# Performance work log

Measured on AMD Instinct MI355X. Metric: run time of the kernel, lower is better.

The kernel has to match this reference:

```python
import jax, jax.numpy as jnp
import numpy as np

B = 128          # graphs
N = 512          # nodes per graph
NT = B * N       # total nodes = 65536
E = NT * 16      # total edges = 1048576
IN = 64
H = 128
OUT = 2
L = 4            # num_layers
RATIO = 0.8


def setup_inputs() -> dict:
    key = jax.random.key(0)
    ks = jax.random.split(key, 20)

    def w(k, shape, fan_in):
        return jax.random.normal(k, shape, jnp.float32) / np.sqrt(fan_in)

    x = jax.random.normal(ks[0], (NT, IN), jnp.float32)
    edge_index = jax.random.randint(ks[1], (2, E), 0, NT, dtype=jnp.int32)
    batch = (jnp.arange(NT) // N).astype(jnp.int32)  # equal-size graphs

    return {
        "x": x,
        "edge_index": edge_index,
        "batch": batch,
        # conv1: GraphConv(IN, H, aggr='mean') -> lin_rel (w/ bias) + lin_root (no bias)
        "W1_rel": w(ks[2], (IN, H), IN),
        "W1_root": w(ks[3], (IN, H), IN),
        "b1": jnp.zeros((H,), jnp.float32),
        # convs[0..2]: GraphConv(H, H, aggr='mean'), stacked
        "Wc_rel": w(ks[4], (L - 1, H, H), H),
        "Wc_root": w(ks[5], (L - 1, H, H), H),
        "bc": jnp.zeros((L - 1, H), jnp.float32),
        # SAGPooling score GNN: GraphConv(H, 1) with default aggr='add'
        "pw_rel": w(ks[6], (H,), H),
        "pw_root": w(ks[7], (H,), H),
        "pb": jnp.zeros((1,), jnp.float32),
        # MLP head
        "lin1_W": w(ks[8], (L * H, H), L * H),
        "lin1_b": jnp.zeros((H,), jnp.float32),
        "lin2_W": w(ks[9], (H, OUT), H),
        "lin2_b": jnp.zeros((OUT,), jnp.float32),
    }


def _graph_conv_mean(x, src, dst, emask, W_rel, W_root, b, n):
    # PyG GraphConv: lin_rel(mean_{j->i} x_j) + lin_root(x_i); masked edges excluded.
    msg = x[src] * emask[:, None]                                  # [E, D] gather
    s = jax.ops.segment_sum(msg, dst, num_segments=n)              # [n, D] scatter-add
    cnt = jax.ops.segment_sum(emask, dst, num_segments=n)          # [n]
    agg = s / jnp.maximum(cnt, 1.0)[:, None]                       # zero for isolated nodes
    return agg @ W_rel + x @ W_root + b


def reference(x, edge_index, batch, W1_rel, W1_root, b1, Wc_rel, Wc_root, bc,
              pw_rel, pw_root, pb, lin1_W, lin1_b, lin2_W, lin2_b):
    src = edge_index[0]
    dst = edge_index[1]
    emask = jnp.ones((E,), jnp.float32)
    n = NT
    npg = N  # nodes per graph (all graphs equal size)

    h = jax.nn.relu(_graph_conv_mean(x, src, dst, emask, W1_rel, W1_root, b1, n))
    xs = [h.reshape(B, npg, H).mean(axis=1)]  # global_mean_pool

    for i in range(L - 1):
        h = jax.nn.relu(_graph_conv_mean(h, src, dst, emask, Wc_rel[i], Wc_root[i], bc[i], n))
        xs.append(h.reshape(B, npg, H).mean(axis=1))
        if i % 2 == 0 and i < L - 2:
            # ---- SAGPooling: score via GraphConv(H,1) with add aggregation ----
            smsg = jax.ops.segment_sum(h[src] * emask[:, None], dst, num_segments=n)
            score = smsg @ pw_rel + h @ pw_root + pb[0]            # [n]
            k = int(np.ceil(RATIO * npg))
            topv, topi = jax.lax.top_k(score.reshape(B, npg), k)   # per-graph top-k
            perm = (jnp.arange(B)[:, None] * npg + topi).reshape(-1)  # global kept ids
            h = h[perm] * jnp.tanh(topv.reshape(-1))[:, None]
            # remap edges; edges touching dropped nodes get masked out
            node_map = jnp.full((n,), -1, jnp.int32).at[perm].set(
                jnp.arange(B * k, dtype=jnp.int32))
            ns, nd = node_map[src], node_map[dst]
            keep = ((ns >= 0) & (nd >= 0)).astype(jnp.float32)
            emask = emask * keep
            src = jnp.where(ns >= 0, ns, 0)
            dst = jnp.where(nd >= 0, nd, 0)
            n = B * k
            npg = k

    xcat = jnp.concatenate(xs, axis=-1)                            # JumpingKnowledge 'cat'
    out = jax.nn.relu(xcat @ lin1_W + lin1_b)
    # dropout is identity in eval mode
    out = out @ lin2_W + lin2_b
    return jax.nn.log_softmax(out, axis=-1)
```

## Files before the change

kernel.cpp:

```cpp
#include <hip/hip_runtime.h>
#include <math.h>

#define NT 65536
#define EE 1048576
#define NB 128
#define KK 410
#define HH 128

typedef short bf16x8 __attribute__((ext_vector_type(8)));
typedef float f32x4 __attribute__((ext_vector_type(4)));
typedef unsigned int u32x4 __attribute__((ext_vector_type(4)));

__device__ __align__(16) unsigned short g_xbs[(size_t)8 * NT * 8];
__device__ __align__(16) unsigned short g_hs1[(size_t)8 * NT * 16];
__device__ __align__(16) unsigned short g_hgs[(size_t)8 * NT * 16];
__device__ __align__(16) unsigned short g_hb2[(size_t)NT * HH];
__device__ __align__(16) unsigned char  g_h8b[(size_t)8 * NT * 16];
__device__ __align__(16) unsigned short g_agg[(size_t)16 * NT * 8];
__device__ __align__(16) unsigned short g_wt1[128 * 128];
__device__ __align__(16) unsigned short g_wtc[3 * 128 * 256];
__device__ __align__(16) unsigned short g_csr1u[EE];
__device__ unsigned short g_keptu[NT];
__device__ unsigned int g_ebuck[EE];
__device__ int g_bcnt[128];
__device__ int g_bbase[129];
__device__ int g_bcur[128];
__device__ int g_nperm[NT];
__device__ float g_trel[NT];
__device__ float g_troot[NT];
__device__ float g_gatef[NT];
__device__ float g_kinv[NT];
__device__ float g_xc4[4 * NB * 4 * 128];
__device__ int g_rows1[NT + 1];

__device__ __forceinline__ unsigned short* wbuf(int id) { return id ? g_wtc : g_wt1; }

__device__ __forceinline__ float b2f(unsigned short u) {
    union { unsigned int i; float f; } v;
    v.i = ((unsigned int)u) << 16;
    return v.f;
}
__device__ __forceinline__ unsigned short f2b(float f) {
    unsigned int x = __float_as_uint(f);
    unsigned int r = x + 0x7fffu + ((x >> 16) & 1u);
    return (unsigned short)(r >> 16);
}
__device__ __forceinline__ unsigned int pk2(float a, float b) {
    return (unsigned int)f2b(a) | ((unsigned int)f2b(b) << 16);
}
__device__ __forceinline__ unsigned int mul2(unsigned int wd, float g) {
    float lo = b2f((unsigned short)(wd & 0xffffu)) * g;
    float hi = b2f((unsigned short)(wd >> 16)) * g;
    return pk2(lo, hi);
}
__device__ __forceinline__ unsigned char enc8(float v) {
    v = fminf(v, 496.0f);
    unsigned int b = __float_as_uint(v * 0x1p-120f);
    unsigned int r = (b + 0x3ffffu + ((b >> 19) & 1u)) >> 19;
    return (unsigned char)r;
}
#define DEC8(u) ((u) ? __uint_as_float(((unsigned int)(u) << 19) + 0x3C000000u) : 0.0f)

__global__ void k_prep(const float* __restrict__ x,
                       const float* __restrict__ W1r, const float* __restrict__ W1o,
                       const float* __restrict__ Wcr, const float* __restrict__ Wco) {
    int tid = blockIdx.x * 256 + threadIdx.x;
    if (tid < 1048576) {
        float4 v = *(const float4*)&x[(size_t)tid * 4];
        unsigned int lo = pk2(v.x, v.y);
        unsigned int hi = pk2(v.z, v.w);
        int node = tid >> 4;
        int sl = (tid & 15) >> 1;
        int of = (tid & 1) * 4;
        *(uint2*)&g_xbs[(((size_t)sl) * NT + node) * 8 + of] = make_uint2(lo, hi);
    } else if (tid < 1048576 + 16384) {
        int r = tid - 1048576;
        int k = r & 127, n = r >> 7;
        float v = (k < 64) ? W1r[k * 128 + n] : W1o[(k - 64) * 128 + n];
        g_wt1[n * 128 + k] = f2b(v);
    } else if (tid < 1048576 + 16384 + 98304) {
        int r = tid - (1048576 + 16384);
        int l = r >> 15;
        int k = r & 255, n = (r >> 8) & 127;
        float v = (k < 128) ? Wcr[l * 16384 + k * 128 + n]
                            : Wco[l * 16384 + (k - 128) * 128 + n];
        g_wtc[l * 32768 + n * 256 + k] = f2b(v);
    } else if (tid < 1048576 + 16384 + 98304 + 128) {
        g_bcnt[tid - (1048576 + 16384 + 98304)] = 0;
    }
}

__global__ __launch_bounds__(256) void k_bhist(const int* __restrict__ dst) {
    __shared__ int h[128];
    if (threadIdx.x < 128) h[threadIdx.x] = 0;
    __syncthreads();
    int e0 = (blockIdx.x * 256 + threadIdx.x) * 4;
    int4 d = *(const int4*)&dst[e0];
    atomicAdd(&h[d.x >> 9], 1);
    atomicAdd(&h[d.y >> 9], 1);
    atomicAdd(&h[d.z >> 9], 1);
    atomicAdd(&h[d.w >> 9], 1);
    __syncthreads();
    if (threadIdx.x < 128 && h[threadIdx.x]) atomicAdd(&g_bcnt[threadIdx.x], h[threadIdx.x]);
}

__global__ __launch_bounds__(128) void k_bscan() {
    __shared__ int s[128];
    int t = threadIdx.x;
    int v = g_bcnt[t];
    s[t] = v;
    __syncthreads();
    for (int off = 1; off < 128; off <<= 1) {
        int u = (t >= off) ? s[t - off] : 0;
        __syncthreads();
        s[t] += u;
        __syncthreads();
    }
    g_bbase[t] = s[t] - v;
    g_bcur[t] = s[t] - v;
    if (t == 127) g_bbase[128] = s[127];
}

__global__ __launch_bounds__(256) void k_bscatter(const int* __restrict__ src,
                                                  const int* __restrict__ dst) {
    __shared__ int h[128];
    __shared__ int base[128];
    if (threadIdx.x < 128) h[threadIdx.x] = 0;
    __syncthreads();
    int e0 = (blockIdx.x * 256 + threadIdx.x) * 4;
    int4 s = *(const int4*)&src[e0];
    int4 d = *(const int4*)&dst[e0];
    int b0 = d.x >> 9, b1 = d.y >> 9, b2 = d.z >> 9, b3 = d.w >> 9;
    atomicAdd(&h[b0], 1);
    atomicAdd(&h[b1], 1);
    atomicAdd(&h[b2], 1);
    atomicAdd(&h[b3], 1);
    __syncthreads();
    if (threadIdx.x < 128) {
        int c = h[threadIdx.x];
        base[threadIdx.x] = c ? atomicAdd(&g_bcur[threadIdx.x], c) : 0;
        h[threadIdx.x] = 0;
    }
    __syncthreads();
    int r0 = atomicAdd(&h[b0], 1);
    g_ebuck[base[b0] + r0] = ((unsigned int)(d.x & 511) << 16) | (unsigned int)s.x;
    int r1 = atomicAdd(&h[b1], 1);
    g_ebuck[base[b1] + r1] = ((unsigned int)(d.y & 511) << 16) | (unsigned int)s.y;
    int r2 = atomicAdd(&h[b2], 1);
    g_ebuck[base[b2] + r2] = ((unsigned int)(d.z & 511) << 16) | (unsigned int)s.z;
    int r3 = atomicAdd(&h[b3], 1);
    g_ebuck[base[b3] + r3] = ((unsigned int)(d.w & 511) << 16) | (unsigned int)s.w;
}

__global__ __launch_bounds__(512) void k_bcsr() {
    __shared__ int hist[512];
    __shared__ int offs[512];
    __shared__ int cur[512];
    int g = blockIdx.x, t = threadIdx.x;
    hist[t] = 0;
    cur[t] = 0;
    __syncthreads();
    int b0 = g_bbase[g], b1 = g_bbase[g + 1];
    for (int e = b0 + t; e < b1; e += 512) {
        unsigned int p = g_ebuck[e];
        atomicAdd(&hist[p >> 16], 1);
    }
    __syncthreads();
    int v = hist[t];
    offs[t] = v;
    __syncthreads();
    for (int off = 1; off < 512; off <<= 1) {
        int u = (t >= off) ? offs[t - off] : 0;
        __syncthreads();
        offs[t] += u;
        __syncthreads();
    }
    int excl = offs[t] - v;
    g_rows1[g * 512 + t] = b0 + excl;
    if (t == 511) g_rows1[g * 512 + 512] = b0 + excl + v;
    __syncthreads();
    offs[t] = excl;
    __syncthreads();
    for (int e = b0 + t; e < b1; e += 512) {
        unsigned int p = g_ebuck[e];
        int dl = p >> 16;
        int r = atomicAdd(&cur[dl], 1);
        g_csr1u[b0 + offs[dl] + r] = (unsigned short)(p & 0xFFFFu);
    }
}

__global__ __launch_bounds__(512) void k_dperm() {
    __shared__ int h[64];
    __shared__ int base[64];
    int g = blockIdx.x, t = threadIdx.x;
    if (t < 64) h[t] = 0;
    __syncthreads();
    int n = g * 512 + t;
    int d = min(g_rows1[n + 1] - g_rows1[n], 63);
    atomicAdd(&h[d], 1);
    __syncthreads();
    if (t == 0) {
        int ss = 0;
        for (int i = 0; i < 64; i++) { base[i] = ss; ss += h[i]; }
    }
    __syncthreads();
    int pos = atomicAdd(&base[d], 1);
    g_nperm[g * 512 + pos] = n;
}

#define ACCP(wd, J) { acc[J] += b2f((unsigned short)((wd) & 0xffffu)); acc[(J) + 1] += b2f((unsigned short)((wd) >> 16)); }
#define ACCQ(q, B) ACCP(q.x, B) ACCP(q.y, (B) + 2) ACCP(q.z, (B) + 4) ACCP(q.w, (B) + 6)

template <int F, int DEN, int FP8>
__global__ __launch_bounds__(256) void k_agg(int srcId) {
    int s = blockIdx.x & 7;
    int idx = (blockIdx.x >> 3) * 256 + threadIdx.x;
    int node = g_nperm[idx];
    const unsigned short* sp = nullptr;
    const unsigned char* sp8 = nullptr;
    if constexpr (FP8) {
        sp8 = g_h8b + (size_t)s * NT * 16;
    } else if constexpr (F == 8) {
        sp = g_xbs + (size_t)s * NT * 8;
    } else {
        sp = (srcId == 0 ? g_hs1 : g_hgs) + (size_t)s * NT * 16;
    }
    int r0 = g_rows1[node], r1 = g_rows1[node + 1];
    float inv;
    if (DEN) {
        inv = g_kinv[node];
    } else {
        int c = r1 - r0;
        inv = 1.0f / (float)(c > 0 ? c : 1);
    }
    constexpr int NA = FP8 ? 16 : F;
    float acc[NA];
#pragma unroll
    for (int i = 0; i < NA; i++) acc[i] = 0.f;

    auto body = [&](int ii) {
        if constexpr (FP8) {
            uint4 w = *(const uint4*)&sp8[(size_t)ii * 16];
            acc[0] += DEC8(w.x & 0xffu);
            acc[1] += DEC8((w.x >> 8) & 0xffu);
            acc[2] += DEC8((w.x >> 16) & 0xffu);
            acc[3] += DEC8(w.x >> 24);
            acc[4] += DEC8(w.y & 0xffu);
            acc[5] += DEC8((w.y >> 8) & 0xffu);
            acc[6] += DEC8((w.y >> 16) & 0xffu);
            acc[7] += DEC8(w.y >> 24);
            acc[8] += DEC8(w.z & 0xffu);
            acc[9] += DEC8((w.z >> 8) & 0xffu);
            acc[10] += DEC8((w.z >> 16) & 0xffu);
            acc[11] += DEC8(w.z >> 24);
            acc[12] += DEC8(w.w & 0xffu);
            acc[13] += DEC8((w.w >> 8) & 0xffu);
            acc[14] += DEC8((w.w >> 16) & 0xffu);
            acc[15] += DEC8(w.w >> 24);
        } else if constexpr (F == 8) {
            uint4 v = *(const uint4*)&sp[(size_t)ii * 8];
            ACCQ(v, 0)
        } else {
            uint4 v = *(const uint4*)&sp[(size_t)ii * 16];
            uint4 v2 = *(const uint4*)&sp[(size_t)ii * 16 + 8];
            ACCQ(v, 0) ACCQ(v2, 8)
        }
    };

    int e = r0;
    for (; e < r1 && (e & 3); e++) body((int)g_csr1u[e]);
    for (; e + 4 <= r1; e += 4) {
        uint2 iv = *(const uint2*)&g_csr1u[e];
        body((int)(iv.x & 0xffffu));
        body((int)(iv.x >> 16));
        body((int)(iv.y & 0xffffu));
        body((int)(iv.y >> 16));
    }
    for (; e < r1; e++) body((int)g_csr1u[e]);

    int gb0 = (NA == 8) ? s : 2 * s;
    u32x4 o;
    o[0] = pk2(acc[0] * inv, acc[1] * inv);
    o[1] = pk2(acc[2] * inv, acc[3] * inv);
    o[2] = pk2(acc[4] * inv, acc[5] * inv);
    o[3] = pk2(acc[6] * inv, acc[7] * inv);
    __builtin_nontemporal_store(o, (u32x4*)&g_agg[((size_t)gb0 * NT + node) * 8]);
    if constexpr (NA == 16) {
        u32x4 o2;
        o2[0] = pk2(acc[8] * inv, acc[9] * inv);
        o2[1] = pk2(acc[10] * inv, acc[11] * inv);
        o2[2] = pk2(acc[12] * inv, acc[13] * inv);
        o2[3] = pk2(acc[14] * inv, acc[15] * inv);
        __builtin_nontemporal_store(o2, (u32x4*)&g_agg[((size_t)(gb0 + 1) * NT + node) * 8]);
    }
}

__global__ __launch_bounds__(256) void k_kinv() {
    int node = blockIdx.x * 256 + threadIdx.x;
    int r0 = g_rows1[node], r1 = g_rows1[node + 1];
    int kc = 0;
    int e = r0;
    for (; e < r1 && (e & 3); e++) kc += (int)g_keptu[g_csr1u[e]];
    for (; e + 4 <= r1; e += 4) {
        uint2 iv = *(const uint2*)&g_csr1u[e];
        kc += (int)g_keptu[iv.x & 0xffffu] + (int)g_keptu[iv.x >> 16]
            + (int)g_keptu[iv.y & 0xffffu] + (int)g_keptu[iv.y >> 16];
    }
    for (; e < r1; e++) kc += (int)g_keptu[g_csr1u[e]];
    g_kinv[node] = 1.0f / (float)(kc > 0 ? kc : 1);
}

__global__ __launch_bounds__(256) void k_gateS() {
    int tid = blockIdx.x * 256 + threadIdx.x;
    int n = tid >> 3, s = tid & 7;
    float g = g_gatef[n];
    const unsigned short* srcp = &g_hb2[(size_t)n * 128 + s * 16];
    uint4 a = *(const uint4*)srcp;
    uint4 b = *(const uint4*)(srcp + 8);
    uint4 oa, ob;
    oa.x = mul2(a.x, g); oa.y = mul2(a.y, g); oa.z = mul2(a.z, g); oa.w = mul2(a.w, g);
    ob.x = mul2(b.x, g); ob.y = mul2(b.y, g); ob.z = mul2(b.z, g); ob.w = mul2(b.w, g);
    unsigned short* d = &g_hgs[((size_t)s * NT + n) * 16];
    *(uint4*)d = oa;
    *(uint4*)(d + 8) = ob;
}

template <int KA, int KB, int MASKED, int DOTS, int ROOTK, int OUTK>
__global__ __launch_bounds__(256) void k_mm(int wsel, int wOfs,
                                            int rootSel,
                                            const float* __restrict__ bias, int sec,
                                            const float* __restrict__ pwr,
                                            const float* __restrict__ pwt) {
    __shared__ float s[128];
    __shared__ unsigned short t16[(OUTK >= 2) ? 128 * 136 : 2];
    const unsigned short* Wt = wbuf(wsel) + wOfs;
    const unsigned short* sb = (ROOTK == 1) ? (rootSel ? g_hgs : g_hs1) : g_xbs;
    int rowbase = blockIdx.x * 128;
    const int K = KA + KB;
    int lane = threadIdx.x & 63;
    int w = threadIdx.x >> 6;
    int n16 = lane & 15, quad = lane >> 4;
    int rowloc = w * 32;
    int rowg = rowbase + rowloc;
    int g = blockIdx.x >> 2, qb = blockIdx.x & 3;
    f32x4 acc[2][8];
#pragma unroll
    for (int rt = 0; rt < 2; rt++)
#pragma unroll
        for (int ct = 0; ct < 8; ct++)
#pragma unroll
            for (int i = 0; i < 4; i++) acc[rt][ct][i] = 0.f;

#pragma unroll
    for (int ks = 0; ks < K / 32; ks++) {
        int k0 = ks * 32;
        bf16x8 a0, a1;
        if (k0 < KA) {
            int fg = (k0 + quad * 8) >> 3;
            a0 = *(const bf16x8*)&g_agg[((size_t)fg * NT + rowg + n16) * 8];
            a1 = *(const bf16x8*)&g_agg[((size_t)fg * NT + rowg + 16 + n16) * 8];
        } else {
            int col = k0 - KA + quad * 8;
            if constexpr (ROOTK == 0) {
                int fg = col >> 3;
                a0 = *(const bf16x8*)&g_xbs[((size_t)fg * NT + rowg + n16) * 8];
                a1 = *(const bf16x8*)&g_xbs[((size_t)fg * NT + rowg + 16 + n16) * 8];
            } else {
                int fg = col >> 4, off = col & 15;
                a0 = *(const bf16x8*)&sb[((size_t)fg * NT + rowg + n16) * 16 + off];
                a1 = *(const bf16x8*)&sb[((size_t)fg * NT + rowg + 16 + n16) * 16 + off];
            }
        }
#pragma unroll
        for (int ct = 0; ct < 8; ct++) {
            bf16x8 b = *(const bf16x8*)&Wt[(size_t)(ct * 16 + n16) * K + k0 + quad * 8];
            acc[0][ct] = __builtin_amdgcn_mfma_f32_16x16x32_bf16(a0, b, acc[0][ct], 0, 0, 0);
            acc[1][ct] = __builtin_amdgcn_mfma_f32_16x16x32_bf16(a1, b, acc[1][ct], 0, 0, 0);
        }
    }

    if (threadIdx.x < 128) s[threadIdx.x] = 0.f;
#pragma unroll
    for (int rt = 0; rt < 2; rt++) {
        float m[4];
#pragma unroll
        for (int i = 0; i < 4; i++) {
            int r = rowg + rt * 16 + quad * 4 + i;
            m[i] = (!MASKED || g_keptu[r]) ? 1.0f : 0.0f;
        }
#pragma unroll
        for (int ct = 0; ct < 8; ct++) {
            int c = ct * 16 + n16;
            float bv = bias[c];
#pragma unroll
            for (int i = 0; i < 4; i++) {
                int r = rowg + rt * 16 + quad * 4 + i;
                float v = fmaxf(acc[rt][ct][i] + bv, 0.f) * m[i];
                acc[rt][ct][i] = v;
                if constexpr (OUTK == 1) g_hb2[(size_t)r * 128 + c] = f2b(v);
                if constexpr (OUTK >= 2) t16[(rowloc + rt * 16 + quad * 4 + i) * 136 + c] = f2b(v);
            }
        }
    }
    __syncthreads();

#pragma unroll
    for (int ct = 0; ct < 8; ct++) {
        float p = 0.f;
#pragma unroll
        for (int rt = 0; rt < 2; rt++)
#pragma unroll
            for (int i = 0; i < 4; i++) p += acc[rt][ct][i];
        p += __shfl_xor(p, 16);
        p += __shfl_xor(p, 32);
        if (quad == 0) atomicAdd(&s[ct * 16 + n16], p);
    }

    if (DOTS) {
        float pr[8], pt[8];
#pragma unroll
        for (int ct = 0; ct < 8; ct++) {
            pr[ct] = pwr[ct * 16 + n16];
            pt[ct] = pwt[ct * 16 + n16];
        }
#pragma unroll
        for (int rt = 0; rt < 2; rt++)
#pragma unroll
            for (int i = 0; i < 4; i++) {
                float dr = 0.f, dt = 0.f;
#pragma unroll
                for (int ct = 0; ct < 8; ct++) {
                    dr += acc[rt][ct][i] * pr[ct];
                    dt += acc[rt][ct][i] * pt[ct];
                }
                dr += __shfl_xor(dr, 1); dt += __shfl_xor(dt, 1);
                dr += __shfl_xor(dr, 2); dt += __shfl_xor(dt, 2);
                dr += __shfl_xor(dr, 4); dt += __shfl_xor(dt, 4);
                dr += __shfl_xor(dr, 8); dt += __shfl_xor(dt, 8);
                if (n16 == 0) {
                    int r = rowg + rt * 16 + quad * 4 + i;
                    g_trel[r] = dr;
                    g_troot[r] = dt;
                }
            }
    }
    __syncthreads();
    if (threadIdx.x < 128)
        g_xc4[((sec * NB + g) * 4 + qb) * 128 + threadIdx.x] = s[threadIdx.x];

    if constexpr (OUTK >= 2) {
        int tid = threadIdx.x;
#pragma unroll
        for (int rep = 0; rep < 8; rep++) {
            int chunk = rep * 256 + tid;
            int s_ = chunk >> 8, rem = chunk & 255;
            int nl = rem >> 1, hf = rem & 1;
            bf16x8 val = *(const bf16x8*)&t16[nl * 136 + s_ * 16 + hf * 8];
            *(bf16x8*)&g_hs1[((size_t)s_ * NT + rowbase + nl) * 16 + hf * 8] = val;
        }
        if constexpr (OUTK == 3) {
#pragma unroll
            for (int rep = 0; rep < 4; rep++) {
                int chunk = rep * 256 + tid;
                int s_ = chunk >> 7, nl = chunk & 127;
                const unsigned short* p = &t16[nl * 136 + s_ * 16];
                unsigned int wq[4];
#pragma unroll
                for (int q = 0; q < 4; q++) {
                    unsigned int c0 = enc8(b2f(p[q * 4 + 0]));
                    unsigned int c1 = enc8(b2f(p[q * 4 + 1]));
                    unsigned int c2 = enc8(b2f(p[q * 4 + 2]));
                    unsigned int c3 = enc8(b2f(p[q * 4 + 3]));
                    wq[q] = c0 | (c1 << 8) | (c2 << 16) | (c3 << 24);
                }
                *(uint4*)&g_h8b[((size_t)s_ * NT + rowbase + nl) * 16] =
                    make_uint4(wq[0], wq[1], wq[2], wq[3]);
            }
        }
    }
}

__global__ __launch_bounds__(256) void k_topk(const float* __restrict__ pb) {
    __shared__ float sv[512];
    __shared__ int si[512];
    int g = blockIdx.x, t = threadIdx.x;
    float pbv = pb[0];
    for (int l = t; l < 512; l += 256) {
        int node = g * 512 + l;
        int r0 = g_rows1[node], r1 = g_rows1[node + 1];
        float s = 0.f;
        int e = r0;
        for (; e + 4 <= r1; e += 4) {
            float s0 = g_trel[g_csr1u[e]];
            float s1 = g_trel[g_csr1u[e + 1]];
            float s2 = g_trel[g_csr1u[e + 2]];
            float s3 = g_trel[g_csr1u[e + 3]];
            s += (s0 + s1) + (s2 + s3);
        }
        for (; e < r1; e++) s += g_trel[g_csr1u[e]];
        sv[l] = s + g_troot[node] + pbv;
        si[l] = l;
    }
    __syncthreads();
    for (int k = 2; k <= 512; k <<= 1) {
        for (int j = k >> 1; j > 0; j >>= 1) {
            for (int i = t; i < 512; i += 256) {
                int p = i ^ j;
                if (p > i) {
                    float va = sv[i], vb = sv[p];
                    int ia = si[i], ib = si[p];
                    bool aFirst = (va > vb) || (va == vb && ia < ib);
                    bool up = ((i & k) == 0);
                    if (up != aFirst) { sv[i] = vb; sv[p] = va; si[i] = ib; si[p] = ia; }
                }
            }
            __syncthreads();
        }
    }
    for (int r = t; r < 512; r += 256) {
        int old = g * 512 + si[r];
        if (r < KK) {
            g_gatef[old] = tanhf(sv[r]);
            g_keptu[old] = 1;
        } else {
            g_gatef[old] = 0.f;
            g_keptu[old] = 0;
        }
    }
}

__global__ __launch_bounds__(128) void k_head(const float* __restrict__ W1, const float* __restrict__ b1,
                                              const float* __restrict__ W2, const float* __restrict__ b2,
                                              float* __restrict__ out) {
    __shared__ float xr[512];
    __shared__ float r0[128], r1[128];
    int g = blockIdx.x, t = threadIdx.x;
    for (int i = t; i < 512; i += 128) {
        int sec = i >> 7, c = i & 127;
        const float* p = &g_xc4[((sec * NB + g) * 4) * 128 + c];
        float v = p[0] + p[128] + p[256] + p[384];
        float inv = (sec < 2) ? (1.0f / 512.0f) : (1.0f / 410.0f);
        xr[i] = v * inv;
    }
    __syncthreads();
    float acc = b1[t];
    for (int k = 0; k < 512; k++) acc += xr[k] * W1[k * 128 + t];
    acc = fmaxf(acc, 0.f);
    r0[t] = acc * W2[t * 2 + 0];
    r1[t] = acc * W2[t * 2 + 1];
    __syncthreads();
    for (int off = 64; off > 0; off >>= 1) {
        if (t < off) { r0[t] += r0[t + off]; r1[t] += r1[t + off]; }
        __syncthreads();
    }
    if (t == 0) {
        float z0 = r0[0] + b2[0], z1 = r1[0] + b2[1];
        float m = fmaxf(z0, z1);
        float l = m + logf(expf(z0 - m) + expf(z1 - m));
        out[g * 2 + 0] = z0 - l;
        out[g * 2 + 1] = z1 - l;
    }
}

extern "C" void kernel_launch(void* const* d_in, const int* in_sizes, int n_in,
                              void* d_out, int out_size, void* d_ws, size_t ws_size,
                              hipStream_t stream) {
    const float* x = (const float*)d_in[0];
    const int* ei = (const int*)d_in[1];
    const int* src = ei;
    const int* dst = ei + EE;
    const float* W1r = (const float*)d_in[3];
    const float* W1o = (const float*)d_in[4];
    const float* b1 = (const float*)d_in[5];
    const float* Wcr = (const float*)d_in[6];
    const float* Wco = (const float*)d_in[7];
    const float* bc = (const float*)d_in[8];
    const float* pwr = (const float*)d_in[9];
    const float* pwt = (const float*)d_in[10];
    const float* pb = (const float*)d_in[11];
    const float* l1W = (const float*)d_in[12];
    const float* l1b = (const float*)d_in[13];
    const float* l2W = (const float*)d_in[14];
    const float* l2b = (const float*)d_in[15];
    float* out = (float*)d_out;

    k_prep<<<(1048576 + 16384 + 98304 + 128 + 255) / 256, 256, 0, stream>>>(x, W1r, W1o, Wcr, Wco);

    k_bhist<<<1024, 256, 0, stream>>>(dst);
    k_bscan<<<1, 128, 0, stream>>>();
    k_bscatter<<<1024, 256, 0, stream>>>(src, dst);
    k_bcsr<<<128, 512, 0, stream>>>();
    k_dperm<<<NB, 512, 0, stream>>>();

    k_agg<8, 0, 0><<<2048, 256, 0, stream>>>(0);
    k_mm<64, 64, 0, 0, 0, 2><<<512, 256, 0, stream>>>(0, 0, 0, b1, 0, pwr, pwt);

    k_agg<16, 0, 0><<<2048, 256, 0, stream>>>(0);
    k_mm<128, 128, 0, 1, 1, 1><<<512, 256, 0, stream>>>(1, 0, 0, bc, 1, pwr, pwt);

    k_topk<<<NB, 256, 0, stream>>>(pb);
    k_kinv<<<NT / 256, 256, 0, stream>>>();
    k_gateS<<<2048, 256, 0, stream>>>();

    k_agg<16, 1, 0><<<2048, 256, 0, stream>>>(1);
    k_mm<128, 128, 1, 0, 1, 3><<<512, 256, 0, stream>>>(1, 32768, 1, bc + 128, 2, pwr, pwt);

    k_agg<16, 1, 1><<<2048, 256, 0, stream>>>(0);
    k_mm<128, 128, 1, 0, 1, 0><<<512, 256, 0, stream>>>(1, 65536, 0, bc + 256, 3, pwr, pwt);

    k_head<<<NB, 128, 0, stream>>>(l1W, l1b, l2W, l2b, out);
}
```

Measured before the change: 531.1 us.

## Sort nodes by degree inside aggregation blocks and split 16-wide rows across two lanes

The separate k_dperm kernel and its global permutation array are removed. Each aggregation block now builds its own degree-sorted node order in shared memory. For the bf16 16-feature aggregation passes, each node row is split across two threads, each loading 8 features, and the grid is doubled. This cuts per-thread register use and serial latency per edge and adds parallelism, at the cost of duplicate CSR index reads per pair of lanes and the in-block sort overhead.

```diff
diff --git a/kernel.cpp b/kernel.cpp
--- a/kernel.cpp
+++ b/kernel.cpp
@@ -25,15 +25,12 @@
 __device__ int g_bcnt[128];
 __device__ int g_bbase[129];
 __device__ int g_bcur[128];
-__device__ int g_nperm[NT];
 __device__ float g_trel[NT];
 __device__ float g_troot[NT];
 __device__ float g_gatef[NT];
 __device__ float g_kinv[NT];
 __device__ float g_xc4[4 * NB * 4 * 128];
 __device__ int g_rows1[NT + 1];
-
-__device__ __forceinline__ unsigned short* wbuf(int id) { return id ? g_wtc : g_wt1; }
 
 __device__ __forceinline__ float b2f(unsigned short u) {
     union { unsigned int i; float f; } v;
@@ -189,33 +186,41 @@
     }
 }
 
-__global__ __launch_bounds__(512) void k_dperm() {
-    __shared__ int h[64];
-    __shared__ int base[64];
-    int g = blockIdx.x, t = threadIdx.x;
-    if (t < 64) h[t] = 0;
-    __syncthreads();
-    int n = g * 512 + t;
-    int d = min(g_rows1[n + 1] - g_rows1[n], 63);
-    atomicAdd(&h[d], 1);
+template <int F, int DEN, int FP8, int LPR>
+__global__ __launch_bounds__(256) void k_agg(int srcId) {
+    constexpr int NPB = 256 / LPR;
+    __shared__ int dh[64];
+    __shared__ int db[64];
+    __shared__ unsigned short sord[NPB];
+    int s = blockIdx.x & 7;
+    int nodebase = (blockIdx.x >> 3) * NPB;
+    int t = threadIdx.x;
+
+    if (t < 64) dh[t] = 0;
+    __syncthreads();
+    int dcap = 0;
+    if (t < NPB) {
+        int n = nodebase + t;
+        dcap = min(g_rows1[n + 1] - g_rows1[n], 63);
+        atomicAdd(&dh[dcap], 1);
+    }
     __syncthreads();
     if (t == 0) {
         int ss = 0;
-        for (int i = 0; i < 64; i++) { base[i] = ss; ss += h[i]; }
-    }
-    __syncthreads();
-    int pos = atomicAdd(&base[d], 1);
-    g_nperm[g * 512 + pos] = n;
-}
-
-#define ACCP(wd, J) { acc[J] += b2f((unsigned short)((wd) & 0xffffu)); acc[(J) + 1] += b2f((unsigned short)((wd) >> 16)); }
-#define ACCQ(q, B) ACCP(q.x, B) ACCP(q.y, (B) + 2) ACCP(q.z, (B) + 4) ACCP(q.w, (B) + 6)
-
-template <int F, int DEN, int FP8>
-__global__ __launch_bounds__(256) void k_agg(int srcId) {
-    int s = blockIdx.x & 7;
-    int idx = (blockIdx.x >> 3) * 256 + threadIdx.x;
-    int node = g_nperm[idx];
+#pragma unroll
+        for (int i = 0; i < 64; i++) { db[i] = ss; ss += dh[i]; }
+    }
+    __syncthreads();
+    if (t < NPB) {
+        int p = atomicAdd(&db[dcap], 1);
+        sord[p] = (unsigned short)t;
+    }
+    __syncthreads();
+
+    int row = sord[t / LPR];
+    int half = (LPR == 2) ? (t & 1) : 0;
+    int node = nodebase + row;
+
     const unsigned short* sp = nullptr;
     const unsigned char* sp8 = nullptr;
     if constexpr (FP8) {
@@ -223,7 +228,7 @@
     } else if constexpr (F == 8) {
         sp = g_xbs + (size_t)s * NT * 8;
     } else {
-        sp = (srcId == 0 ? g_hs1 : g_hgs) + (size_t)s * NT * 16;
+        sp = (srcId == 0 ? g_hs1 : g_hgs) + (size_t)s * NT * 16 + half * 8;
     }
     int r0 = g_rows1[node], r1 = g_rows1[node + 1];
     float inv;
@@ -233,11 +238,12 @@
         int c = r1 - r0;
         inv = 1.0f / (float)(c > 0 ? c : 1);
     }
-    constexpr int NA = FP8 ? 16 : F;
+    constexpr int NA = FP8 ? 16 : 8;
     float acc[NA];
 #pragma unroll
     for (int i = 0; i < NA; i++) acc[i] = 0.f;
 
+#define ACCP(wd, J) { acc[J] += b2f((unsigned short)((wd) & 0xffffu)); acc[(J) + 1] += b2f((unsigned short)((wd) >> 16)); }
     auto body = [&](int ii) {
         if constexpr (FP8) {
             uint4 w = *(const uint4*)&sp8[(size_t)ii * 16];
@@ -259,13 +265,13 @@
             acc[15] += DEC8(w.w >> 24);
         } else if constexpr (F == 8) {
             uint4 v = *(const uint4*)&sp[(size_t)ii * 8];
-            ACCQ(v, 0)
+            ACCP(v.x, 0) ACCP(v.y, 2) ACCP(v.z, 4) ACCP(v.w, 6)
         } else {
             uint4 v = *(const uint4*)&sp[(size_t)ii * 16];
-            uint4 v2 = *(const uint4*)&sp[(size_t)ii * 16 + 8];
-            ACCQ(v, 0) ACCQ(v2, 8)
+            ACCP(v.x, 0) ACCP(v.y, 2) ACCP(v.z, 4) ACCP(v.w, 6)
         }
     };
+#undef ACCP
 
     int e = r0;
     for (; e < r1 && (e & 3); e++) body((int)g_csr1u[e]);
@@ -278,20 +284,20 @@
     }
     for (; e < r1; e++) body((int)g_csr1u[e]);
 
-    int gb0 = (NA == 8) ? s : 2 * s;
+    int gb0 = (F == 8) ? s : (2 * s + half);
     u32x4 o;
     o[0] = pk2(acc[0] * inv, acc[1] * inv);
     o[1] = pk2(acc[2] * inv, acc[3] * inv);
     o[2] = pk2(acc[4] * inv, acc[5] * inv);
     o[3] = pk2(acc[6] * inv, acc[7] * inv);
     __builtin_nontemporal_store(o, (u32x4*)&g_agg[((size_t)gb0 * NT + node) * 8]);
-    if constexpr (NA == 16) {
+    if constexpr (FP8) {
         u32x4 o2;
         o2[0] = pk2(acc[8] * inv, acc[9] * inv);
         o2[1] = pk2(acc[10] * inv, acc[11] * inv);
         o2[2] = pk2(acc[12] * inv, acc[13] * inv);
         o2[3] = pk2(acc[14] * inv, acc[15] * inv);
-        __builtin_nontemporal_store(o2, (u32x4*)&g_agg[((size_t)(gb0 + 1) * NT + node) * 8]);
+        __builtin_nontemporal_store(o2, (u32x4*)&g_agg[((size_t)(2 * s + 1) * NT + node) * 8]);
     }
 }
 
@@ -333,7 +339,7 @@
                                             const float* __restrict__ pwt) {
     __shared__ float s[128];
     __shared__ unsigned short t16[(OUTK >= 2) ? 128 * 136 : 2];
-    const unsigned short* Wt = wbuf(wsel) + wOfs;
+    const unsigned short* Wt = (wsel ? g_wtc : g_wt1) + wOfs;
     const unsigned short* sb = (ROOTK == 1) ? (rootSel ? g_hgs : g_hs1) : g_xbs;
     int rowbase = blockIdx.x * 128;
     const int K = KA + KB;
@@ -590,22 +596,21 @@
     k_bscan<<<1, 128, 0, stream>>>();
     k_bscatter<<<1024, 256, 0, stream>>>(src, dst);
     k_bcsr<<<128, 512, 0, stream>>>();
-    k_dperm<<<NB, 512, 0, stream>>>();
-
-    k_agg<8, 0, 0><<<2048, 256, 0, stream>>>(0);
+
+    k_agg<8, 0, 0, 1><<<2048, 256, 0, stream>>>(0);
     k_mm<64, 64, 0, 0, 0, 2><<<512, 256, 0, stream>>>(0, 0, 0, b1, 0, pwr, pwt);
 
-    k_agg<16, 0, 0><<<2048, 256, 0, stream>>>(0);
+    k_agg<16, 0, 0, 2><<<4096, 256, 0, stream>>>(0);
     k_mm<128, 128, 0, 1, 1, 1><<<512, 256, 0, stream>>>(1, 0, 0, bc, 1, pwr, pwt);
 
     k_topk<<<NB, 256, 0, stream>>>(pb);
     k_kinv<<<NT / 256, 256, 0, stream>>>();
     k_gateS<<<2048, 256, 0, stream>>>();
 
-    k_agg<16, 1, 0><<<2048, 256, 0, stream>>>(1);
+    k_agg<16, 1, 0, 2><<<4096, 256, 0, stream>>>(1);
     k_mm<128, 128, 1, 0, 1, 3><<<512, 256, 0, stream>>>(1, 32768, 1, bc + 128, 2, pwr, pwt);
 
-    k_agg<16, 1, 1><<<2048, 256, 0, stream>>>(0);
+    k_agg<16, 1, 1, 1><<<2048, 256, 0, stream>>>(0);
     k_mm<128, 128, 1, 0, 1, 0><<<512, 256, 0, stream>>>(1, 65536, 0, bc + 256, 3, pwr, pwt);
 
     k_head<<<NB, 128, 0, stream>>>(l1W, l1b, l2W, l2b, out);
```

Result: faster. 513.6 us (-3.3%).

## Prune CSR to kept neighbours after pooling and store aggregates in degree-sorted order

Applied to the files above, without the earlier changes.

A new prune kernel replaces the kept-count kernel. It builds a compacted CSR that holds only neighbours surviving top-k pooling, so the layer-3/4 aggregation no longer gathers feature rows that are masked out anyway. Nodes are re-sorted by kept degree to balance the load. Aggregation kernels now write outputs at the permuted index, giving coalesced stores, and the matmul reads through a rank map. The catch is a serial per-thread prune loop with uncoalesced writes, plus indirect loads in the matmul A operand.

```diff
diff --git a/kernel.cpp b/kernel.cpp
--- a/kernel.cpp
+++ b/kernel.cpp
@@ -20,20 +20,23 @@
 __device__ __align__(16) unsigned short g_wt1[128 * 128];
 __device__ __align__(16) unsigned short g_wtc[3 * 128 * 256];
 __device__ __align__(16) unsigned short g_csr1u[EE];
+__device__ __align__(16) unsigned short g_csr2u[EE];
 __device__ unsigned short g_keptu[NT];
 __device__ unsigned int g_ebuck[EE];
 __device__ int g_bcnt[128];
 __device__ int g_bbase[129];
 __device__ int g_bcur[128];
-__device__ int g_nperm[NT];
+__device__ int g_kdeg[NT];
+__device__ int g_perm1[NT];
+__device__ int g_perm2[NT];
+__device__ int g_rank1[NT];
+__device__ int g_rank2[NT];
 __device__ float g_trel[NT];
 __device__ float g_troot[NT];
 __device__ float g_gatef[NT];
 __device__ float g_kinv[NT];
 __device__ float g_xc4[4 * NB * 4 * 128];
 __device__ int g_rows1[NT + 1];
-
-__device__ __forceinline__ unsigned short* wbuf(int id) { return id ? g_wtc : g_wt1; }
 
 __device__ __forceinline__ float b2f(unsigned short u) {
     union { unsigned int i; float f; } v;
@@ -201,45 +204,74 @@
     __syncthreads();
     if (t == 0) {
         int ss = 0;
+#pragma unroll
         for (int i = 0; i < 64; i++) { base[i] = ss; ss += h[i]; }
     }
     __syncthreads();
     int pos = atomicAdd(&base[d], 1);
-    g_nperm[g * 512 + pos] = n;
-}
-
-#define ACCP(wd, J) { acc[J] += b2f((unsigned short)((wd) & 0xffffu)); acc[(J) + 1] += b2f((unsigned short)((wd) >> 16)); }
-#define ACCQ(q, B) ACCP(q.x, B) ACCP(q.y, (B) + 2) ACCP(q.z, (B) + 4) ACCP(q.w, (B) + 6)
-
-template <int F, int DEN, int FP8>
-__global__ __launch_bounds__(256) void k_agg(int srcId) {
+    g_perm1[g * 512 + pos] = n;
+    g_rank1[n] = pos;
+}
+
+__global__ __launch_bounds__(512) void k_prune() {
+    __shared__ int h[64];
+    __shared__ int base[64];
+    int g = blockIdx.x, t = threadIdx.x;
+    int n = g * 512 + t;
+    int r0 = g_rows1[n], r1 = g_rows1[n + 1];
+    int kc = 0;
+    for (int e = r0; e < r1; e++) {
+        unsigned short sidx = g_csr1u[e];
+        if (g_keptu[sidx]) { g_csr2u[r0 + kc] = sidx; kc++; }
+    }
+    g_kdeg[n] = kc;
+    g_kinv[n] = 1.0f / (float)(kc > 0 ? kc : 1);
+    if (t < 64) h[t] = 0;
+    __syncthreads();
+    int d = min(kc, 63);
+    atomicAdd(&h[d], 1);
+    __syncthreads();
+    if (t == 0) {
+        int ss = 0;
+#pragma unroll
+        for (int i = 0; i < 64; i++) { base[i] = ss; ss += h[i]; }
+    }
+    __syncthreads();
+    int pos = atomicAdd(&base[d], 1);
+    g_perm2[g * 512 + pos] = n;
+    g_rank2[n] = pos;
+}
+
+template <int MODE>
+__global__ __launch_bounds__(256) void k_agg() {
     int s = blockIdx.x & 7;
     int idx = (blockIdx.x >> 3) * 256 + threadIdx.x;
-    int node = g_nperm[idx];
-    const unsigned short* sp = nullptr;
-    const unsigned char* sp8 = nullptr;
-    if constexpr (FP8) {
-        sp8 = g_h8b + (size_t)s * NT * 16;
-    } else if constexpr (F == 8) {
-        sp = g_xbs + (size_t)s * NT * 8;
-    } else {
-        sp = (srcId == 0 ? g_hs1 : g_hgs) + (size_t)s * NT * 16;
-    }
-    int r0 = g_rows1[node], r1 = g_rows1[node + 1];
+    int node = (MODE >= 2) ? g_perm2[idx] : g_perm1[idx];
+    const unsigned short* csr = (MODE >= 2) ? g_csr2u : g_csr1u;
+    int r0 = g_rows1[node];
+    int r1 = (MODE >= 2) ? (r0 + g_kdeg[node]) : g_rows1[node + 1];
     float inv;
-    if (DEN) {
+    if constexpr (MODE >= 2) {
         inv = g_kinv[node];
     } else {
         int c = r1 - r0;
         inv = 1.0f / (float)(c > 0 ? c : 1);
     }
-    constexpr int NA = FP8 ? 16 : F;
+    constexpr int NA = (MODE == 0) ? 8 : 16;
     float acc[NA];
 #pragma unroll
     for (int i = 0; i < NA; i++) acc[i] = 0.f;
 
+    const unsigned short* sp = nullptr;
+    const unsigned char* sp8 = nullptr;
+    if constexpr (MODE == 0) sp = g_xbs + (size_t)s * NT * 8;
+    else if constexpr (MODE == 1) sp = g_hs1 + (size_t)s * NT * 16;
+    else if constexpr (MODE == 2) sp = g_hgs + (size_t)s * NT * 16;
+    else sp8 = g_h8b + (size_t)s * NT * 16;
+
+#define ACCP(wd, J) { acc[J] += b2f((unsigned short)((wd) & 0xffffu)); acc[(J) + 1] += b2f((unsigned short)((wd) >> 16)); }
     auto body = [&](int ii) {
-        if constexpr (FP8) {
+        if constexpr (MODE == 3) {
             uint4 w = *(const uint4*)&sp8[(size_t)ii * 16];
             acc[0] += DEC8(w.x & 0xffu);
             acc[1] += DEC8((w.x >> 8) & 0xffu);
@@ -257,57 +289,45 @@
             acc[13] += DEC8((w.w >> 8) & 0xffu);
             acc[14] += DEC8((w.w >> 16) & 0xffu);
             acc[15] += DEC8(w.w >> 24);
-        } else if constexpr (F == 8) {
+        } else if constexpr (MODE == 0) {
             uint4 v = *(const uint4*)&sp[(size_t)ii * 8];
-            ACCQ(v, 0)
+            ACCP(v.x, 0) ACCP(v.y, 2) ACCP(v.z, 4) ACCP(v.w, 6)
         } else {
             uint4 v = *(const uint4*)&sp[(size_t)ii * 16];
             uint4 v2 = *(const uint4*)&sp[(size_t)ii * 16 + 8];
-            ACCQ(v, 0) ACCQ(v2, 8)
+            ACCP(v.x, 0) ACCP(v.y, 2) ACCP(v.z, 4) ACCP(v.w, 6)
+            ACCP(v2.x, 8) ACCP(v2.y, 10) ACCP(v2.z, 12) ACCP(v2.w, 14)
         }
     };
+#undef ACCP
 
     int e = r0;
-    for (; e < r1 && (e & 3); e++) body((int)g_csr1u[e]);
+    for (; e < r1 && (e & 3); e++) body((int)csr[e]);
     for (; e + 4 <= r1; e += 4) {
-        uint2 iv = *(const uint2*)&g_csr1u[e];
+        uint2 iv = *(const uint2*)&csr[e];
         body((int)(iv.x & 0xffffu));
         body((int)(iv.x >> 16));
         body((int)(iv.y & 0xffffu));
         body((int)(iv.y >> 16));
     }
-    for (; e < r1; e++) body((int)g_csr1u[e]);
-
-    int gb0 = (NA == 8) ? s : 2 * s;
+    for (; e < r1; e++) body((int)csr[e]);
+
     u32x4 o;
     o[0] = pk2(acc[0] * inv, acc[1] * inv);
     o[1] = pk2(acc[2] * inv, acc[3] * inv);
     o[2] = pk2(acc[4] * inv, acc[5] * inv);
     o[3] = pk2(acc[6] * inv, acc[7] * inv);
-    __builtin_nontemporal_store(o, (u32x4*)&g_agg[((size_t)gb0 * NT + node) * 8]);
-    if constexpr (NA == 16) {
+    if constexpr (MODE == 0) {
+        __builtin_nontemporal_store(o, (u32x4*)&g_agg[((size_t)s * NT + idx) * 8]);
+    } else {
+        __builtin_nontemporal_store(o, (u32x4*)&g_agg[((size_t)(2 * s) * NT + idx) * 8]);
         u32x4 o2;
         o2[0] = pk2(acc[8] * inv, acc[9] * inv);
         o2[1] = pk2(acc[10] * inv, acc[11] * inv);
         o2[2] = pk2(acc[12] * inv, acc[13] * inv);
         o2[3] = pk2(acc[14] * inv, acc[15] * inv);
-        __builtin_nontemporal_store(o2, (u32x4*)&g_agg[((size_t)(gb0 + 1) * NT + node) * 8]);
-    }
-}
-
-__global__ __launch_bounds__(256) void k_kinv() {
-    int node = blockIdx.x * 256 + threadIdx.x;
-    int r0 = g_rows1[node], r1 = g_rows1[node + 1];
-    int kc = 0;
-    int e = r0;
-    for (; e < r1 && (e & 3); e++) kc += (int)g_keptu[g_csr1u[e]];
-    for (; e + 4 <= r1; e += 4) {
-        uint2 iv = *(const uint2*)&g_csr1u[e];
-        kc += (int)g_keptu[iv.x & 0xffffu] + (int)g_keptu[iv.x >> 16]
-            + (int)g_keptu[iv.y & 0xffffu] + (int)g_keptu[iv.y >> 16];
-    }
-    for (; e < r1; e++) kc += (int)g_keptu[g_csr1u[e]];
-    g_kinv[node] = 1.0f / (float)(kc > 0 ? kc : 1);
+        __builtin_nontemporal_store(o2, (u32x4*)&g_agg[((size_t)(2 * s + 1) * NT + idx) * 8]);
+    }
 }
 
 __global__ __launch_bounds__(256) void k_gateS() {
@@ -326,15 +346,15 @@
 }
 
 template <int KA, int KB, int MASKED, int DOTS, int ROOTK, int OUTK>
-__global__ __launch_bounds__(256) void k_mm(int wsel, int wOfs,
-                                            int rootSel,
+__global__ __launch_bounds__(256) void k_mm(int wsel, int wOfs, int rootSel, int rksel,
                                             const float* __restrict__ bias, int sec,
                                             const float* __restrict__ pwr,
                                             const float* __restrict__ pwt) {
     __shared__ float s[128];
     __shared__ unsigned short t16[(OUTK >= 2) ? 128 * 136 : 2];
-    const unsigned short* Wt = wbuf(wsel) + wOfs;
+    const unsigned short* Wt = (wsel ? g_wtc : g_wt1) + wOfs;
     const unsigned short* sb = (ROOTK == 1) ? (rootSel ? g_hgs : g_hs1) : g_xbs;
+    const int* rankp = rksel ? g_rank2 : g_rank1;
     int rowbase = blockIdx.x * 128;
     const int K = KA + KB;
     int lane = threadIdx.x & 63;
@@ -343,6 +363,9 @@
     int rowloc = w * 32;
     int rowg = rowbase + rowloc;
     int g = blockIdx.x >> 2, qb = blockIdx.x & 3;
+    int row0 = rowg + n16, row1 = rowg + 16 + n16;
+    int ia0 = (row0 & ~511) | rankp[row0];
+    int ia1 = (row1 & ~511) | rankp[row1];
     f32x4 acc[2][8];
 #pragma unroll
     for (int rt = 0; rt < 2; rt++)
@@ -357,18 +380,18 @@
         bf16x8 a0, a1;
         if (k0 < KA) {
             int fg = (k0 + quad * 8) >> 3;
-            a0 = *(const bf16x8*)&g_agg[((size_t)fg * NT + rowg + n16) * 8];
-            a1 = *(const bf16x8*)&g_agg[((size_t)fg * NT + rowg + 16 + n16) * 8];
+            a0 = *(const bf16x8*)&g_agg[((size_t)fg * NT + ia0) * 8];
+            a1 = *(const bf16x8*)&g_agg[((size_t)fg * NT + ia1) * 8];
         } else {
             int col = k0 - KA + quad * 8;
             if constexpr (ROOTK == 0) {
                 int fg = col >> 3;
-                a0 = *(const bf16x8*)&g_xbs[((size_t)fg * NT + rowg + n16) * 8];
-                a1 = *(const bf16x8*)&g_xbs[((size_t)fg * NT + rowg + 16 + n16) * 8];
+                a0 = *(const bf16x8*)&g_xbs[((size_t)fg * NT + row0) * 8];
+                a1 = *(const bf16x8*)&g_xbs[((size_t)fg * NT + row1) * 8];
             } else {
                 int fg = col >> 4, off = col & 15;
-                a0 = *(const bf16x8*)&sb[((size_t)fg * NT + rowg + n16) * 16 + off];
-                a1 = *(const bf16x8*)&sb[((size_t)fg * NT + rowg + 16 + n16) * 16 + off];
+                a0 = *(const bf16x8*)&sb[((size_t)fg * NT + row0) * 16 + off];
+                a1 = *(const bf16x8*)&sb[((size_t)fg * NT + row1) * 16 + off];
             }
         }
 #pragma unroll
@@ -592,21 +615,21 @@
     k_bcsr<<<128, 512, 0, stream>>>();
     k_dperm<<<NB, 512, 0, stream>>>();
 
-    k_agg<8, 0, 0><<<2048, 256, 0, stream>>>(0);
-    k_mm<64, 64, 0, 0, 0, 2><<<512, 256, 0, stream>>>(0, 0, 0, b1, 0, pwr, pwt);
-
-    k_agg<16, 0, 0><<<2048, 256, 0, stream>>>(0);
-    k_mm<128, 128, 0, 1, 1, 1><<<512, 256, 0, stream>>>(1, 0, 0, bc, 1, pwr, pwt);
+    k_agg<0><<<2048, 256, 0, stream>>>();
+    k_mm<64, 64, 0, 0, 0, 2><<<512, 256, 0, stream>>>(0, 0, 0, 0, b1, 0, pwr, pwt);
+
+    k_agg<1><<<2048, 256, 0, stream>>>();
+    k_mm<128, 128, 0, 1, 1, 1><<<512, 256, 0, stream>>>(1, 0, 0, 0, bc, 1, pwr, pwt);
 
     k_topk<<<NB, 256, 0, stream>>>(pb);
-    k_kinv<<<NT / 256, 256, 0, stream>>>();
+    k_prune<<<NB, 512, 0, stream>>>();
     k_gateS<<<2048, 256, 0, stream>>>();
 
-    k_agg<16, 1, 0><<<2048, 256, 0, stream>>>(1);
-    k_mm<128, 128, 1, 0, 1, 3><<<512, 256, 0, stream>>>(1, 32768, 1, bc + 128, 2, pwr, pwt);
-
-    k_agg<16, 1, 1><<<2048, 256, 0, stream>>>(0);
-    k_mm<128, 128, 1, 0, 1, 0><<<512, 256, 0, stream>>>(1, 65536, 0, bc + 256, 3, pwr, pwt);
+    k_agg<2><<<2048, 256, 0, stream>>>();
+    k_mm<128, 128, 1, 0, 1, 3><<<512, 256, 0, stream>>>(1, 32768, 1, 1, bc + 128, 2, pwr, pwt);
+
+    k_agg<3><<<2048, 256, 0, stream>>>();
+    k_mm<128, 128, 1, 0, 1, 0><<<512, 256, 0, stream>>>(1, 65536, 0, 1, bc + 256, 3, pwr, pwt);
 
     k_head<<<NB, 128, 0, stream>>>(l1W, l1b, l2W, l2b, out);
 }
```

Result: slower. 550.1 us (+3.6%).
